# Kernel optimization log

Hardware: AMD Instinct MI355X
Metric: run time of the kernel (lower is better)

Reference implementation:

```python
import jax, jax.numpy as jnp
import numpy as np

D = 2048; HQ = 16; HKV = 4; HD = 128
E = 8; F = 2048; FS = 11008; TOPK = 2
B = 2; S = 1024
EPS = 1e-6
NEG = -1e9


def setup_inputs() -> dict:
    key = jax.random.key(0)
    ks = jax.random.split(key, 16)
    p = lambda k, shape: jax.random.normal(k, shape, jnp.float32) * 0.02
    # rotary tables (rotate-half convention): [S, HD]
    pos = jnp.arange(S, dtype=jnp.float32)[:, None]
    inv = 1.0 / (10000.0 ** (jnp.arange(0, HD, 2, dtype=jnp.float32) / HD))
    ang = pos * inv[None, :]
    cos = jnp.concatenate([jnp.cos(ang), jnp.cos(ang)], axis=-1)
    sin = jnp.concatenate([jnp.sin(ang), jnp.sin(ang)], axis=-1)
    return dict(
        x=jax.random.normal(ks[0], (B, S, D), jnp.float32),
        rope_cos=cos, rope_sin=sin,
        attn_norm_w=jnp.ones((D,), jnp.float32),
        ffn_norm_w=jnp.ones((D,), jnp.float32),
        wq=p(ks[1], (D, HQ * HD)), bq=jnp.zeros((HQ * HD,), jnp.float32),
        wk=p(ks[2], (D, HKV * HD)), bk=jnp.zeros((HKV * HD,), jnp.float32),
        wv=p(ks[3], (D, HKV * HD)), bv=jnp.zeros((HKV * HD,), jnp.float32),
        wo=p(ks[4], (HQ * HD, D)),
        router_w=p(ks[5], (D, E)),
        w_gate=p(ks[6], (E, D, F)), w_up=p(ks[7], (E, D, F)), w_down=p(ks[8], (E, F, D)),
        ws_gate=p(ks[9], (D, FS)), ws_up=p(ks[10], (D, FS)), ws_down=p(ks[11], (FS, D)),
    )


def rmsnorm(x, w):
    return x * jax.lax.rsqrt(jnp.mean(x * x, axis=-1, keepdims=True) + EPS) * w


def rotate_half(x):
    x1, x2 = jnp.split(x, 2, axis=-1)
    return jnp.concatenate([-x2, x1], axis=-1)


def reference(x, rope_cos, rope_sin, attn_norm_w, ffn_norm_w,
              wq, bq, wk, bk, wv, bv, wo, router_w,
              w_gate, w_up, w_down, ws_gate, ws_up, ws_down):
    b, s, d = x.shape
    # ---- attention sublayer ----
    h = rmsnorm(x, attn_norm_w)
    q = (h @ wq + bq).reshape(b, s, HQ, HD)
    k = (h @ wk + bk).reshape(b, s, HKV, HD)
    v = (h @ wv + bv).reshape(b, s, HKV, HD)
    cos = rope_cos[None, :, None, :]
    sin = rope_sin[None, :, None, :]
    q = q * cos + rotate_half(q) * sin
    k = k * cos + rotate_half(k) * sin
    rep = HQ // HKV
    k = jnp.repeat(k, rep, axis=2)   # [b,s,HQ,HD]
    v = jnp.repeat(v, rep, axis=2)
    scores = jnp.einsum('bqhd,bkhd->bhqk', q, k) / np.sqrt(HD).astype(np.float32)
    causal = jnp.tril(jnp.ones((s, s), bool))
    scores = jnp.where(causal[None, None], scores, NEG)
    attn = jax.nn.softmax(scores, axis=-1)
    o = jnp.einsum('bhqk,bkhd->bqhd', attn, v).reshape(b, s, HQ * HD) @ wo
    new_k, new_v = k, v
    x = x + o
    # ---- MoE sublayer ----
    hn = rmsnorm(x, ffn_norm_w).reshape(b * s, d)   # [T,D]
    logits = hn @ router_w                           # [T,E]
    probs = jax.nn.softmax(logits, axis=-1)
    topv, topi = jax.lax.top_k(probs, TOPK)          # [T,K]
    topv = topv / jnp.sum(topv, axis=-1, keepdims=True)
    onehot = jax.nn.one_hot(topi, E, dtype=hn.dtype)  # [T,K,E]
    wdense = jnp.einsum('tke,tk->te', onehot, topv)   # sparse combine weights [T,E]
    g = jnp.einsum('td,edf->tef', hn, w_gate)
    u = jnp.einsum('td,edf->tef', hn, w_up)
    y = jnp.einsum('tef,efd->ted', jax.nn.silu(g) * u, w_down)
    routed = jnp.einsum('ted,te->td', y, wdense)
    shared = (jax.nn.silu(hn @ ws_gate) * (hn @ ws_up)) @ ws_down
    moe = (routed + shared).reshape(b, s, d)
    # load-balancing aux loss (Switch/Mixtral convention)
    frac = jnp.mean(onehot, axis=(0, 1))             # fraction dispatched per expert
    pmean = jnp.mean(probs, axis=0)
    aux_loss = E * jnp.sum(frac * pmean)
    out = x + moe
    return out, (new_k, new_v), aux_loss
```

## Files before the change

kernel.cpp:

```cpp
#include <hip/hip_runtime.h>

typedef unsigned short u16;
typedef unsigned int u32;
typedef unsigned long long u64;
typedef __attribute__((ext_vector_type(4))) unsigned short u16x4;
typedef __attribute__((ext_vector_type(8))) unsigned short u16x8;
typedef __attribute__((ext_vector_type(4))) float f32x4;
typedef __attribute__((ext_vector_type(8))) __bf16 bf16x8;

#define DD 2048
#define TT 2048
#define FSH 11008

__device__ __forceinline__ float bf2f(u16 u) {
  union { u32 i; float f; } v; v.i = ((u32)u) << 16; return v.f;
}
__device__ __forceinline__ u16 f2bf(float f) {
  union { float f; u32 i; } v; v.f = f;
  u32 r = v.i + 0x7fffu + ((v.i >> 16) & 1u);
  return (u16)(r >> 16);
}
__device__ __forceinline__ void gld16(const void* g, void* l) {
  __builtin_amdgcn_global_load_lds((const __attribute__((address_space(1))) void*)g,
                                   (__attribute__((address_space(3))) void*)l, 16, 0, 0);
}

#define MFMA16(d, a, b) d = __builtin_amdgcn_mfma_f32_16x16x32_bf16(a, b, d, 0, 0, 0)

__global__ __launch_bounds__(256) void rmsnorm_k(const float* __restrict__ x,
                                                 const float* __restrict__ w,
                                                 u16* __restrict__ out) {
  const int t = threadIdx.x;
  const float* xr = x + (size_t)blockIdx.x * DD;
  float4 a = *(const float4*)(xr + t * 8);
  float4 b = *(const float4*)(xr + t * 8 + 4);
  float ss = a.x*a.x + a.y*a.y + a.z*a.z + a.w*a.w
           + b.x*b.x + b.y*b.y + b.z*b.z + b.w*b.w;
#pragma unroll
  for (int m = 1; m < 64; m <<= 1) ss += __shfl_xor(ss, m);
  __shared__ float red[4];
  if ((t & 63) == 0) red[t >> 6] = ss;
  __syncthreads();
  float sc = rsqrtf((red[0] + red[1] + red[2] + red[3]) * (1.f / DD) + 1e-6f);
  float4 wa = *(const float4*)(w + t * 8);
  float4 wb = *(const float4*)(w + t * 8 + 4);
  u16x8 o;
  o[0] = f2bf(a.x * sc * wa.x); o[1] = f2bf(a.y * sc * wa.y);
  o[2] = f2bf(a.z * sc * wa.z); o[3] = f2bf(a.w * sc * wa.w);
  o[4] = f2bf(b.x * sc * wb.x); o[5] = f2bf(b.y * sc * wb.y);
  o[6] = f2bf(b.z * sc * wb.z); o[7] = f2bf(b.w * sc * wb.w);
  *(u16x8*)(out + (size_t)blockIdx.x * DD + t * 8) = o;
}

__global__ __launch_bounds__(256) void transp_k(const float* __restrict__ W,
                                                u16* __restrict__ Wt, int R, int C) {
  __shared__ u16 tile[64 * 80];
  const size_t msz = (size_t)R * C;
  const float* Wm = W + msz * blockIdx.z;
  u16* Wtm = Wt + msz * blockIdx.z;
  const int t = threadIdx.x;
  const int n0 = blockIdx.x * 64, k0 = blockIdx.y * 64;
#pragma unroll
  for (int p = 0; p < 4; ++p) {
    const int kk = (t >> 4) + p * 16;
    const int nn = (t & 15) * 4;
    float4 v = *(const float4*)(Wm + (size_t)(k0 + kk) * C + n0 + nn);
    tile[(nn + 0) * 80 + kk] = f2bf(v.x);
    tile[(nn + 1) * 80 + kk] = f2bf(v.y);
    tile[(nn + 2) * 80 + kk] = f2bf(v.z);
    tile[(nn + 3) * 80 + kk] = f2bf(v.w);
  }
  __syncthreads();
#pragma unroll
  for (int p = 0; p < 2; ++p) {
    const int n = (t >> 3) + p * 32;
    const int c = t & 7;
    u16x8 v = *(const u16x8*)(tile + n * 80 + c * 8);
    *(u16x8*)(Wtm + (size_t)(n0 + n) * R + k0 + c * 8) = v;
  }
}

template <int EPI, bool EXPERT, bool INDIR, bool SPLITK>
__global__ __launch_bounds__(256) void gemm2(
    const u16* __restrict__ A, const u16* __restrict__ Bt, void* __restrict__ Cp,
    const void* __restrict__ aux, const float* __restrict__ slotw,
    const int* __restrict__ slot_tok, const int* __restrict__ tiletab,
    int M, int N, int K, int Kc) {
  __shared__ u16 lA[128 * 32];
  __shared__ u16 lB[128 * 32];
  const int t = threadIdx.x, w = t >> 6, l = t & 63;
  const int n0 = blockIdx.x * 128;
  int m0;
  if constexpr (EXPERT) {
    const int ntil = tiletab[0];
    if ((int)blockIdx.y >= ntil) return;
    const int e = tiletab[1 + blockIdx.y * 2];
    m0 = tiletab[2 + blockIdx.y * 2];
    Bt += (size_t)e * N * K;
  } else {
    m0 = blockIdx.y * 128;
  }
  int kbase = 0, KC = K;
  if constexpr (SPLITK) { kbase = blockIdx.z * Kc; KC = Kc; }
  const int srow = w * 16 + (l >> 2);
  const int scol = (l & 3) * 8;
  const int r0 = m0 + srow, r1 = m0 + srow + 64;
  const u16 *ag0, *ag1;
  if constexpr (INDIR) {
    ag0 = A + (size_t)slot_tok[r0] * K + scol + kbase;
    ag1 = A + (size_t)slot_tok[r1] * K + scol + kbase;
  } else {
    ag0 = A + (size_t)r0 * K + scol + kbase;
    ag1 = A + (size_t)r1 * K + scol + kbase;
  }
  const u16* bg0 = Bt + (size_t)(n0 + srow) * K + scol + kbase;
  const u16* bg1 = Bt + (size_t)(n0 + srow + 64) * K + scol + kbase;
  u16* la = lA + w * 512;
  u16* lb = lB + w * 512;
  const int l15 = l & 15, l4 = l >> 4;
  const int wm = w >> 1, wn = w & 1;
  const int fa = (wm * 64 + l15) * 32 + l4 * 8;
  const int fb = (wn * 64 + l15) * 32 + l4 * 8;
  f32x4 acc[4][4] = {};
  for (int ko = 0; ko < KC; ko += 32) {
    __syncthreads();
    gld16(ag0 + ko, la);
    gld16(ag1 + ko, la + 2048);
    gld16(bg0 + ko, lb);
    gld16(bg1 + ko, lb + 2048);
    asm volatile("s_waitcnt vmcnt(0)" ::: "memory");
    __syncthreads();
    bf16x8 af[4], bf[4];
#pragma unroll
    for (int i = 0; i < 4; ++i) {
      af[i] = *(const bf16x8*)(lA + fa + i * 512);
      bf[i] = *(const bf16x8*)(lB + fb + i * 512);
    }
#pragma unroll
    for (int mi = 0; mi < 4; ++mi)
#pragma unroll
      for (int ni = 0; ni < 4; ++ni)
        MFMA16(acc[mi][ni], af[mi], bf[ni]);
  }
  float* Cf = (float*)Cp;
  if constexpr (SPLITK) Cf += (size_t)blockIdx.z * M * N;
#pragma unroll
  for (int mi = 0; mi < 4; ++mi) {
#pragma unroll
    for (int r = 0; r < 4; ++r) {
      const int row = m0 + wm * 64 + mi * 16 + l4 * 4 + r;
#pragma unroll
      for (int ni = 0; ni < 4; ++ni) {
        const int col = n0 + wn * 64 + ni * 16 + l15;
        const size_t idx = (size_t)row * N + col;
        const float v = acc[mi][ni][r];
        if constexpr (EPI == 0) Cf[idx] = v;
        else if constexpr (EPI == 2) ((u16*)Cp)[idx] = f2bf(v);
        else if constexpr (EPI == 3) {
          const float g = bf2f(((const u16*)aux)[idx]);
          ((u16*)Cp)[idx] = f2bf(v * g / (1.f + __expf(-g)));
        } else {
          ((u16*)Cp)[idx] = f2bf(slotw[row] * v);
        }
      }
    }
  }
}

template <int EPI, bool SPLITK>
__global__ __launch_bounds__(512, 2) void gemm8(
    const u16* __restrict__ A, const u16* __restrict__ Bt, void* __restrict__ Cp,
    const u16* __restrict__ aux, int M, int N, int K, int Kc) {
  __shared__ char lds[131072];
  const int t = threadIdx.x, w = t >> 6, l = t & 63;
  const int gx = gridDim.x;
  const int nwg = gx * gridDim.y;
  int wg = blockIdx.y * gx + blockIdx.x;
  wg = (wg & 7) * (nwg >> 3) + (wg >> 3);
  const int n0 = (wg % gx) * 256;
  const int m0 = (wg / gx) * 256;
  int kbase = 0, KC = K;
  if constexpr (SPLITK) {
    kbase = blockIdx.z * Kc;
    const int rem = K - kbase;
    KC = rem < Kc ? rem : Kc;
  }
  const int ktiles = KC >> 6;
  const int wm = w >> 2, wn = w & 3;
  const int l15 = l & 15, l4 = l >> 4;
  const int sro = l >> 3, sc = l & 7;

  const u16* sgp[2][2][2];
  u32 sdo[2][2][2];
#pragma unroll
  for (int isB = 0; isB < 2; ++isB)
#pragma unroll
    for (int h = 0; h < 2; ++h)
#pragma unroll
      for (int i = 0; i < 2; ++i) {
        const int q = i * 8 + w;
        const int r0 = isB ? (((q >> 2) << 6) + h * 32 + (q & 3) * 8)
                           : (((q & 8) << 4) + h * 64 + (q & 7) * 8);
        const int r = r0 + sro;
        const int cl = sc ^ (r & 7);
        const u16* base = isB ? (Bt + (size_t)(n0 + r) * K) : (A + (size_t)(m0 + r) * K);
        sgp[isB][h][i] = base + kbase + cl * 8;
        sdo[isB][h][i] = (u32)(isB * 32768 + r0 * 128);
      }
  auto stage = [&](int b, int isB, int h, int kt) {
    const int kk = kt < ktiles ? kt : ktiles - 1;
#pragma unroll
    for (int i = 0; i < 2; ++i)
      gld16(sgp[isB][h][i] + kk * 64, lds + b * 65536 + sdo[isB][h][i]);
  };
  auto ldA = [&](int b, int mi, int ks) {
    const int row = wm * 128 + mi * 16 + l15;
    const int ch = (ks * 4 + l4) ^ (row & 7);
    return *(const bf16x8*)(lds + b * 65536 + row * 128 + ch * 16);
  };
  auto ldB = [&](int b, int ni, int ks) {
    const int row = wn * 64 + ni * 16 + l15;
    const int ch = (ks * 4 + l4) ^ (row & 7);
    return *(const bf16x8*)(lds + b * 65536 + 32768 + row * 128 + ch * 16);
  };

  f32x4 acc[8][4] = {};
  bf16x8 aR[4][2], b0[2][2], b1[2][2];

  stage(0, 0, 0, 0); stage(0, 1, 0, 0); stage(0, 1, 1, 0); stage(0, 0, 1, 0);
  stage(1, 0, 0, 1); stage(1, 1, 1, 1); stage(1, 0, 1, 1);
  asm volatile("s_waitcnt vmcnt(6)" ::: "memory");
  __builtin_amdgcn_s_barrier();

  for (int kt = 0; kt < ktiles; kt += 2) {
#pragma unroll
    for (int mi = 0; mi < 4; ++mi) { aR[mi][0] = ldA(0, mi, 0); aR[mi][1] = ldA(0, mi, 1); }
#pragma unroll
    for (int ni = 0; ni < 2; ++ni) { b0[ni][0] = ldB(0, ni, 0); b0[ni][1] = ldB(0, ni, 1); }
    stage(1, 1, 0, kt + 1);
    __builtin_amdgcn_s_barrier();
    asm volatile("s_waitcnt lgkmcnt(0)" ::: "memory");
    __builtin_amdgcn_s_setprio(1);
#pragma unroll
    for (int mi = 0; mi < 4; ++mi)
#pragma unroll
      for (int ni = 0; ni < 2; ++ni) {
        MFMA16(acc[mi][ni], aR[mi][0], b0[ni][0]);
        MFMA16(acc[mi][ni], aR[mi][1], b0[ni][1]);
      }
    __builtin_amdgcn_s_setprio(0);
    __builtin_amdgcn_s_barrier();
#pragma unroll
    for (int ni = 0; ni < 2; ++ni) { b1[ni][0] = ldB(0, ni + 2, 0); b1[ni][1] = ldB(0, ni + 2, 1); }
    stage(0, 0, 0, kt + 2);
    __builtin_amdgcn_s_barrier();
    asm volatile("s_waitcnt lgkmcnt(0)" ::: "memory");
    __builtin_amdgcn_s_setprio(1);
#pragma unroll
    for (int mi = 0; mi < 4; ++mi)
#pragma unroll
      for (int ni = 0; ni < 2; ++ni) {
        MFMA16(acc[mi][ni + 2], aR[mi][0], b1[ni][0]);
        MFMA16(acc[mi][ni + 2], aR[mi][1], b1[ni][1]);
      }
    __builtin_amdgcn_s_setprio(0);
    __builtin_amdgcn_s_barrier();
#pragma unroll
    for (int mi = 0; mi < 4; ++mi) { aR[mi][0] = ldA(0, mi + 4, 0); aR[mi][1] = ldA(0, mi + 4, 1); }
    stage(0, 1, 1, kt + 2);
    __builtin_amdgcn_s_barrier();
    asm volatile("s_waitcnt lgkmcnt(0)" ::: "memory");
    __builtin_amdgcn_s_setprio(1);
#pragma unroll
    for (int mi = 0; mi < 4; ++mi)
#pragma unroll
      for (int ni = 0; ni < 2; ++ni) {
        MFMA16(acc[mi + 4][ni + 2], aR[mi][0], b1[ni][0]);
        MFMA16(acc[mi + 4][ni + 2], aR[mi][1], b1[ni][1]);
      }
    __builtin_amdgcn_s_setprio(0);
    __builtin_amdgcn_s_barrier();
    stage(0, 0, 1, kt + 2);
    __builtin_amdgcn_s_barrier();
    __builtin_amdgcn_s_setprio(1);
#pragma unroll
    for (int mi = 0; mi < 4; ++mi)
#pragma unroll
      for (int ni = 0; ni < 2; ++ni) {
        MFMA16(acc[mi + 4][ni], aR[mi][0], b0[ni][0]);
        MFMA16(acc[mi + 4][ni], aR[mi][1], b0[ni][1]);
      }
    __builtin_amdgcn_s_setprio(0);
    asm volatile("s_waitcnt vmcnt(6)" ::: "memory");
    __builtin_amdgcn_s_barrier();
#pragma unroll
    for (int mi = 0; mi < 4; ++mi) { aR[mi][0] = ldA(1, mi, 0); aR[mi][1] = ldA(1, mi, 1); }
#pragma unroll
    for (int ni = 0; ni < 2; ++ni) { b0[ni][0] = ldB(1, ni, 0); b0[ni][1] = ldB(1, ni, 1); }
    stage(0, 1, 0, kt + 2);
    __builtin_amdgcn_s_barrier();
    asm volatile("s_waitcnt lgkmcnt(0)" ::: "memory");
    __builtin_amdgcn_s_setprio(1);
#pragma unroll
    for (int mi = 0; mi < 4; ++mi)
#pragma unroll
      for (int ni = 0; ni < 2; ++ni) {
        MFMA16(acc[mi][ni], aR[mi][0], b0[ni][0]);
        MFMA16(acc[mi][ni], aR[mi][1], b0[ni][1]);
      }
    __builtin_amdgcn_s_setprio(0);
    __builtin_amdgcn_s_barrier();
#pragma unroll
    for (int ni = 0; ni < 2; ++ni) { b1[ni][0] = ldB(1, ni + 2, 0); b1[ni][1] = ldB(1, ni + 2, 1); }
    stage(1, 0, 0, kt + 3);
    __builtin_amdgcn_s_barrier();
    asm volatile("s_waitcnt lgkmcnt(0)" ::: "memory");
    __builtin_amdgcn_s_setprio(1);
#pragma unroll
    for (int mi = 0; mi < 4; ++mi)
#pragma unroll
      for (int ni = 0; ni < 2; ++ni) {
        MFMA16(acc[mi][ni + 2], aR[mi][0], b1[ni][0]);
        MFMA16(acc[mi][ni + 2], aR[mi][1], b1[ni][1]);
      }
    __builtin_amdgcn_s_setprio(0);
    __builtin_amdgcn_s_barrier();
#pragma unroll
    for (int mi = 0; mi < 4; ++mi) { aR[mi][0] = ldA(1, mi + 4, 0); aR[mi][1] = ldA(1, mi + 4, 1); }
    stage(1, 1, 1, kt + 3);
    __builtin_amdgcn_s_barrier();
    asm volatile("s_waitcnt lgkmcnt(0)" ::: "memory");
    __builtin_amdgcn_s_setprio(1);
#pragma unroll
    for (int mi = 0; mi < 4; ++mi)
#pragma unroll
      for (int ni = 0; ni < 2; ++ni) {
        MFMA16(acc[mi + 4][ni + 2], aR[mi][0], b1[ni][0]);
        MFMA16(acc[mi + 4][ni + 2], aR[mi][1], b1[ni][1]);
      }
    __builtin_amdgcn_s_setprio(0);
    __builtin_amdgcn_s_barrier();
    stage(1, 0, 1, kt + 3);
    __builtin_amdgcn_s_barrier();
    __builtin_amdgcn_s_setprio(1);
#pragma unroll
    for (int mi = 0; mi < 4; ++mi)
#pragma unroll
      for (int ni = 0; ni < 2; ++ni) {
        MFMA16(acc[mi + 4][ni], aR[mi][0], b0[ni][0]);
        MFMA16(acc[mi + 4][ni], aR[mi][1], b0[ni][1]);
      }
    __builtin_amdgcn_s_setprio(0);
    asm volatile("s_waitcnt vmcnt(6)" ::: "memory");
    __builtin_amdgcn_s_barrier();
  }

  u16* C16 = (u16*)Cp;
  float* Cf = (float*)Cp;
  if constexpr (EPI == 10) C16 += (size_t)blockIdx.z * ((size_t)M * N);
  if constexpr (EPI == 11) Cf += (size_t)blockIdx.z * ((size_t)M * N);
#pragma unroll
  for (int mi = 0; mi < 8; ++mi)
#pragma unroll
    for (int rr = 0; rr < 4; ++rr) {
      const int row = m0 + wm * 128 + mi * 16 + l4 * 4 + rr;
#pragma unroll
      for (int ni = 0; ni < 4; ++ni) {
        const int col = n0 + wn * 64 + ni * 16 + l15;
        const size_t idx = (size_t)row * N + col;
        const float v = acc[mi][ni][rr];
        if constexpr (EPI == 11) {
          Cf[idx] = v;
        } else if constexpr (EPI == 3) {
          const float g = bf2f(aux[idx]);
          C16[idx] = f2bf(v * g / (1.f + __expf(-g)));
        } else {
          C16[idx] = f2bf(v);
        }
      }
    }
}

template <int NP, bool ADDB>
__global__ __launch_bounds__(256) void red_k(float* __restrict__ dst,
                                             const float* __restrict__ base,
                                             const float* __restrict__ parts,
                                             int mn4) {
  const int i = blockIdx.x * 256 + threadIdx.x;
  float4 s;
  if constexpr (ADDB) s = ((const float4*)base)[i];
  else { s.x = s.y = s.z = s.w = 0.f; }
#pragma unroll
  for (int p = 0; p < NP; ++p) {
    const float4 v = ((const float4*)parts)[(size_t)p * mn4 + i];
    s.x += v.x; s.y += v.y; s.z += v.z; s.w += v.w;
  }
  ((float4*)dst)[i] = s;
}

__global__ __launch_bounds__(256) void redbf_k(float* __restrict__ dst,
                                               const float* __restrict__ base,
                                               const u16* __restrict__ parts) {
  const int i = blockIdx.x * 256 + threadIdx.x;
  float s[8];
  const float* bp = base + (size_t)i * 8;
#pragma unroll
  for (int j = 0; j < 8; ++j) s[j] = bp[j];
#pragma unroll
  for (int p = 0; p < 4; ++p) {
    u16x8 v = ((const u16x8*)parts)[(size_t)p * 524288 + i];
#pragma unroll
    for (int j = 0; j < 8; ++j) s[j] += bf2f(v[j]);
  }
  float* dp = dst + (size_t)i * 8;
#pragma unroll
  for (int j = 0; j < 8; ++j) dp[j] = s[j];
}

__global__ __launch_bounds__(256) void rope_k(
    const float* __restrict__ qkv, const float* __restrict__ cosb, const float* __restrict__ sinb,
    const float* __restrict__ bq, const float* __restrict__ bk, const float* __restrict__ bv,
    u16* __restrict__ QR, u16* __restrict__ KR, u16* __restrict__ VB,
    float* __restrict__ NK, float* __restrict__ NV) {
  const int s = blockIdx.x, b = blockIdx.y, t = threadIdx.x;
  const size_t tok = (size_t)b * 1024 + s;
  const float* row = qkv + tok * 3072;
  const float* cr = cosb + s * 128;
  const float* sr = sinb + s * 128;
  for (int i = t; i < 1024; i += 256) {
    const int h = i >> 6, d = i & 63;
    const float v1 = row[h * 128 + d] + bq[h * 128 + d];
    const float v2 = row[h * 128 + d + 64] + bq[h * 128 + d + 64];
    const float o1 = v1 * cr[d] - v2 * sr[d];
    const float o2 = v2 * cr[d + 64] + v1 * sr[d + 64];
    const size_t qb = (((size_t)(b * 16 + h)) * 1024 + s) * 128;
    QR[qb + d] = f2bf(o1);
    QR[qb + d + 64] = f2bf(o2);
  }
  {
    const int h = t >> 6, d = t & 63;
    const float v1 = row[2048 + h * 128 + d] + bk[h * 128 + d];
    const float v2 = row[2048 + h * 128 + d + 64] + bk[h * 128 + d + 64];
    const float o1 = v1 * cr[d] - v2 * sr[d];
    const float o2 = v2 * cr[d + 64] + v1 * sr[d + 64];
    const size_t kb = (((size_t)(b * 4 + h)) * 1024 + s) * 128;
    KR[kb + d] = f2bf(o1);
    KR[kb + d + 64] = f2bf(o2);
    const size_t ob = tok * 2048;
#pragma unroll
    for (int rep = 0; rep < 4; ++rep) {
      NK[ob + (h * 4 + rep) * 128 + d] = o1;
      NK[ob + (h * 4 + rep) * 128 + d + 64] = o2;
    }
  }
  for (int i = t; i < 512; i += 256) {
    const int h = i >> 7, d = i & 127;
    const float v = row[2560 + i] + bv[i];
    VB[(((size_t)(b * 4 + h)) * 1024 + s) * 128 + d] = f2bf(v);
    const size_t ob = tok * 2048;
#pragma unroll
    for (int rep = 0; rep < 4; ++rep) NV[ob + (h * 4 + rep) * 128 + d] = v;
  }
}

__global__ __launch_bounds__(256) void attn_k(const u16* __restrict__ Q,
                                              const u16* __restrict__ Kc,
                                              const u16* __restrict__ Vc,
                                              u16* __restrict__ O) {
  const int qt = blockIdx.x, h = blockIdx.y, b = blockIdx.z;
  const int t = threadIdx.x, w = t >> 6, l = t & 63;
  const int kvh = h >> 2;
  __shared__ u16 Ks[64 * 128];
  __shared__ u16 Vt[128 * 66];
  __shared__ u16 Ps[4][16 * 68];
  const int l15 = l & 15, l4 = l >> 4;
  bf16x8 qf[4];
  {
    const u16* qb = Q + (((size_t)(b * 16 + h)) * 1024 + qt * 64 + w * 16 + l15) * 128 + l4 * 8;
#pragma unroll
    for (int c = 0; c < 4; ++c) qf[c] = *(const bf16x8*)(qb + c * 32);
  }
  float m_run[4] = {-1e30f, -1e30f, -1e30f, -1e30f};
  float l_run[4] = {0.f, 0.f, 0.f, 0.f};
  f32x4 accO[8] = {};
  const size_t kvbase = ((size_t)(b * 4 + kvh)) * 1024 * 128;
  const int ntiles = qt + 1;
  for (int kt = 0; kt < ntiles; ++kt) {
    __syncthreads();
    {
      const int key = t >> 2;
      const u16* kg = Kc + kvbase + (size_t)(kt * 64 + key) * 128;
      const u16* vg = Vc + kvbase + (size_t)(kt * 64 + key) * 128;
      const int sw = (key & 7) << 4;
#pragma unroll
      for (int p = 0; p < 4; ++p) {
        const int ch = (t & 3) * 4 + p;
        *(u16x8*)((char*)Ks + key * 256 + ((ch * 16) ^ sw)) = *(const u16x8*)(kg + ch * 8);
        const int d0 = ch * 8;
        u16x8 vv = *(const u16x8*)(vg + d0);
#pragma unroll
        for (int j = 0; j < 8; ++j) Vt[(d0 + j) * 66 + key] = vv[j];
      }
    }
    __syncthreads();
    f32x4 sf[4] = {};
#pragma unroll
    for (int nf = 0; nf < 4; ++nf) {
      const int keyl = nf * 16 + l15;
      const int sw = (keyl & 7) << 4;
      const char* kbase = (const char*)Ks + keyl * 256;
#pragma unroll
      for (int c = 0; c < 4; ++c) {
        bf16x8 kf = *(const bf16x8*)(kbase + ((c * 64 + l4 * 16) ^ sw));
        sf[nf] = __builtin_amdgcn_mfma_f32_16x16x32_bf16(qf[c], kf, sf[nf], 0, 0, 0);
      }
    }
    const int qg0 = qt * 64 + w * 16 + l4 * 4;
    float alpha[4];
#pragma unroll
    for (int r = 0; r < 4; ++r) {
      const int qg = qg0 + r;
      float tm = -1e30f;
#pragma unroll
      for (int nf = 0; nf < 4; ++nf) {
        const int kg = kt * 64 + nf * 16 + l15;
        float sv = sf[nf][r] * 0.088388347648318447f;
        sv = (kg <= qg) ? sv : -1e30f;
        sf[nf][r] = sv;
        tm = fmaxf(tm, sv);
      }
#pragma unroll
      for (int mm = 1; mm < 16; mm <<= 1) tm = fmaxf(tm, __shfl_xor(tm, mm));
      const float mn = fmaxf(m_run[r], tm);
      alpha[r] = __expf(m_run[r] - mn);
      m_run[r] = mn;
      float rs = 0.f;
#pragma unroll
      for (int nf = 0; nf < 4; ++nf) {
        const float p = __expf(sf[nf][r] - mn);
        sf[nf][r] = p;
        rs += p;
      }
#pragma unroll
      for (int mm = 1; mm < 16; mm <<= 1) rs += __shfl_xor(rs, mm);
      l_run[r] = l_run[r] * alpha[r] + rs;
    }
#pragma unroll
    for (int nf = 0; nf < 8; ++nf)
#pragma unroll
      for (int r = 0; r < 4; ++r) accO[nf][r] *= alpha[r];
#pragma unroll
    for (int nf = 0; nf < 4; ++nf)
#pragma unroll
      for (int r = 0; r < 4; ++r)
        Ps[w][(l4 * 4 + r) * 68 + nf * 16 + l15] = f2bf(sf[nf][r]);
    __syncthreads();
#pragma unroll
    for (int kc = 0; kc < 2; ++kc) {
      const u16* pb = &Ps[w][0] + l15 * 68 + kc * 32 + l4 * 8;
      union { u16x4 q[2]; bf16x8 v; } pu;
      pu.q[0] = *(const u16x4*)pb;
      pu.q[1] = *(const u16x4*)(pb + 4);
#pragma unroll
      for (int nf = 0; nf < 8; ++nf) {
        const int dd = nf * 16 + l15;
        const u16* vp = &Vt[0] + dd * 66 + kc * 32 + l4 * 8;
        union { u32 u[4]; bf16x8 v; } vu;
        vu.u[0] = *(const u32*)(vp);
        vu.u[1] = *(const u32*)(vp + 2);
        vu.u[2] = *(const u32*)(vp + 4);
        vu.u[3] = *(const u32*)(vp + 6);
        accO[nf] = __builtin_amdgcn_mfma_f32_16x16x32_bf16(pu.v, vu.v, accO[nf], 0, 0, 0);
      }
    }
  }
  const int qg0 = qt * 64 + w * 16 + l4 * 4;
#pragma unroll
  for (int nf = 0; nf < 8; ++nf) {
    const int dd = nf * 16 + l15;
#pragma unroll
    for (int r = 0; r < 4; ++r) {
      const float o = accO[nf][r] / l_run[r];
      O[((size_t)(b * 1024 + qg0 + r)) * 2048 + h * 128 + dd] = f2bf(o);
    }
  }
}

__global__ __launch_bounds__(256) void router_k(
    const float* __restrict__ x2, const float* __restrict__ wn, const float* __restrict__ rw,
    int* __restrict__ topi2, float* __restrict__ topw2,
    int* __restrict__ counts, u64* __restrict__ pmean) {
  const int t = threadIdx.x, w = t >> 6, l = t & 63;
  const int tok = blockIdx.x * 4 + w;
  __shared__ int lc[8];
  __shared__ u64 lp[8];
  if (t < 8) { lc[t] = 0; lp[t] = 0ull; }
  __syncthreads();
  const float* xr = x2 + (size_t)tok * DD;
  float ss = 0.f;
#pragma unroll
  for (int i = 0; i < 8; ++i) {
    float4 v = *(const float4*)(xr + l * 32 + i * 4);
    ss += v.x * v.x + v.y * v.y + v.z * v.z + v.w * v.w;
  }
#pragma unroll
  for (int m = 1; m < 64; m <<= 1) ss += __shfl_xor(ss, m);
  const float sc = rsqrtf(ss * (1.f / DD) + 1e-6f);
  float acc[8] = {};
  for (int i = 0; i < 32; ++i) {
    const int d = l * 32 + i;
    const float hv = xr[d] * sc * wn[d];
    float4 r0 = *(const float4*)(rw + d * 8);
    float4 r1 = *(const float4*)(rw + d * 8 + 4);
    acc[0] += hv * r0.x; acc[1] += hv * r0.y; acc[2] += hv * r0.z; acc[3] += hv * r0.w;
    acc[4] += hv * r1.x; acc[5] += hv * r1.y; acc[6] += hv * r1.z; acc[7] += hv * r1.w;
  }
#pragma unroll
  for (int m = 1; m < 64; m <<= 1)
#pragma unroll
    for (int e = 0; e < 8; ++e) acc[e] += __shfl_xor(acc[e], m);
  if (l == 0) {
    float mx = acc[0];
#pragma unroll
    for (int e = 1; e < 8; ++e) mx = fmaxf(mx, acc[e]);
    float p[8], sum = 0.f;
#pragma unroll
    for (int e = 0; e < 8; ++e) { p[e] = __expf(acc[e] - mx); sum += p[e]; }
    const float inv = 1.f / sum;
#pragma unroll
    for (int e = 0; e < 8; ++e) p[e] *= inv;
    int e0 = 0; float v0 = p[0];
#pragma unroll
    for (int e = 1; e < 8; ++e) if (p[e] > v0) { v0 = p[e]; e0 = e; }
    int e1 = (e0 == 0) ? 1 : 0; float v1 = p[e1];
#pragma unroll
    for (int e = 0; e < 8; ++e) if (e != e0 && p[e] > v1) { v1 = p[e]; e1 = e; }
    const float wsum = v0 + v1;
    topi2[tok * 2] = e0; topi2[tok * 2 + 1] = e1;
    topw2[tok * 2] = v0 / wsum; topw2[tok * 2 + 1] = v1 / wsum;
    atomicAdd(&lc[e0], 1); atomicAdd(&lc[e1], 1);
#pragma unroll
    for (int e = 0; e < 8; ++e) atomicAdd(&lp[e], (u64)((double)p[e] * 4294967296.0));
  }
  __syncthreads();
  if (t < 8) {
    if (lc[t]) atomicAdd(&counts[t], lc[t]);
    if (lp[t]) atomicAdd(&pmean[t], lp[t]);
  }
}

__global__ __launch_bounds__(256) void zero_k(int* __restrict__ counts, u64* __restrict__ pmean,
                                              int* __restrict__ slot_tok, float* __restrict__ slot_w) {
  const int i = blockIdx.x * 256 + threadIdx.x;
  if (i < 5120) { slot_tok[i] = 0; slot_w[i] = 0.f; }
  if (i < 8) { counts[i] = 0; pmean[i] = 0ull; }
}

__global__ void scan_k(const int* __restrict__ counts, int* __restrict__ cursors,
                       int* __restrict__ tiletab, const u64* __restrict__ pmean,
                       float* __restrict__ auxout) {
  if (threadIdx.x == 0) {
    int off = 0, nt = 0;
    double aux = 0.0;
    for (int e = 0; e < 8; ++e) {
      cursors[e] = off;
      const int c = counts[e];
      const int nte = (c + 127) >> 7;
      for (int i = 0; i < nte; ++i) {
        tiletab[1 + nt * 2] = e;
        tiletab[2 + nt * 2] = off + i * 128;
        ++nt;
      }
      off += nte * 128;
      const double pm = ((double)pmean[e] / 4294967296.0) / 2048.0;
      aux += ((double)c / 4096.0) * pm;
    }
    tiletab[0] = nt;
    *auxout = (float)(8.0 * aux);
  }
}

__global__ __launch_bounds__(256) void assign_k(const int* __restrict__ topi2,
                                                const float* __restrict__ topw2,
                                                int* __restrict__ cursors,
                                                int* __restrict__ slot_tok,
                                                float* __restrict__ slot_w,
                                                int* __restrict__ tok_slot) {
  const int tok = blockIdx.x * 256 + threadIdx.x;
#pragma unroll
  for (int j = 0; j < 2; ++j) {
    const int e = topi2[tok * 2 + j];
    const int s = atomicAdd(&cursors[e], 1);
    slot_tok[s] = tok;
    slot_w[s] = topw2[tok * 2 + j];
    tok_slot[tok * 2 + j] = s;
  }
}

__global__ __launch_bounds__(256) void final_k(float* __restrict__ out,
                                               const u16* __restrict__ routed,
                                               const int* __restrict__ tok_slot) {
  const int tok = blockIdx.x, t = threadIdx.x;
  const int s0 = tok_slot[tok * 2], s1 = tok_slot[tok * 2 + 1];
  u16x8 a = ((const u16x8*)(routed + (size_t)s0 * DD))[t];
  u16x8 b = ((const u16x8*)(routed + (size_t)s1 * DD))[t];
  float* o = out + (size_t)tok * DD + t * 8;
  float4 o0 = *(const float4*)o;
  float4 o1 = *(const float4*)(o + 4);
  o0.x += bf2f(a[0]) + bf2f(b[0]); o0.y += bf2f(a[1]) + bf2f(b[1]);
  o0.z += bf2f(a[2]) + bf2f(b[2]); o0.w += bf2f(a[3]) + bf2f(b[3]);
  o1.x += bf2f(a[4]) + bf2f(b[4]); o1.y += bf2f(a[5]) + bf2f(b[5]);
  o1.z += bf2f(a[6]) + bf2f(b[6]); o1.w += bf2f(a[7]) + bf2f(b[7]);
  *(float4*)o = o0;
  *(float4*)(o + 4) = o1;
}

extern "C" void kernel_launch(void* const* d_in, const int* in_sizes, int n_in,
                              void* d_out, int out_size, void* d_ws, size_t ws_size,
                              hipStream_t stream) {
  (void)in_sizes; (void)n_in; (void)out_size; (void)ws_size;
  const float* x    = (const float*)d_in[0];
  const float* rc   = (const float*)d_in[1];
  const float* rs   = (const float*)d_in[2];
  const float* anw  = (const float*)d_in[3];
  const float* fnw  = (const float*)d_in[4];
  const float* wq   = (const float*)d_in[5];
  const float* bq   = (const float*)d_in[6];
  const float* wk   = (const float*)d_in[7];
  const float* bk   = (const float*)d_in[8];
  const float* wv   = (const float*)d_in[9];
  const float* bv   = (const float*)d_in[10];
  const float* wo   = (const float*)d_in[11];
  const float* rw   = (const float*)d_in[12];
  const float* wg   = (const float*)d_in[13];
  const float* wu   = (const float*)d_in[14];
  const float* wd   = (const float*)d_in[15];
  const float* wsg  = (const float*)d_in[16];
  const float* wsu  = (const float*)d_in[17];
  const float* wsd  = (const float*)d_in[18];

  const size_t MB = (size_t)1 << 20;
  char* ws = (char*)d_ws;
  float* X2  = (float*)(ws + 0);
  u16*   HN  = (u16*)(ws + 16 * MB);
  char*  SM  = ws + 24 * MB;
  char*  AR  = ws + 25 * MB;

  int*   CNT   = (int*)(SM);
  u64*   PM    = (u64*)(SM + 64);
  int*   CURS  = (int*)(SM + 256);
  int*   TILT  = (int*)(SM + 512);
  int*   TOPI  = (int*)(SM + 4096);
  float* TOPW  = (float*)(SM + 40960);
  int*   STOK  = (int*)(SM + 73728);
  float* SW    = (float*)(SM + 98304);
  int*   TSLOT = (int*)(SM + 131072);

  u16*   H      = (u16*)(AR);
  u16*   WTQ    = (u16*)(AR + 8 * MB);
  float* PARTSQ = (float*)(AR + 20 * MB);
  float* QKVF   = (float*)(AR + 68 * MB);
  u16*   QR    = (u16*)(AR);
  u16*   KR    = (u16*)(AR + 8 * MB);
  u16*   VBb   = (u16*)(AR + 10 * MB);
  u16*   ATTNO = (u16*)(AR + 12 * MB);
  u16*   WTO    = (u16*)(AR + 20 * MB);
  float* PARTSW = (float*)(AR + 28 * MB);
  u16*   WTS    = (u16*)(AR);
  u16*   G      = (u16*)(AR + 44 * MB);
  u16*   PARTSD = (u16*)(AR + 88 * MB);
  u16*   WTE    = (u16*)(AR);
  u16*   GEXP   = (u16*)(AR + 64 * MB);
  u16*   ROUTED = (u16*)(AR + 84 * MB);

  float* out  = (float*)d_out;
  float* NK   = out + 4194304;
  float* NV   = out + 2 * 4194304;
  float* AUXO = out + 3 * 4194304;

  const dim3 b256(256);
  const dim3 b512(512);

  rmsnorm_k<<<TT, b256, 0, stream>>>(x, anw, H);
  transp_k<<<dim3(32, 32, 1), b256, 0, stream>>>(wq, WTQ, 2048, 2048);
  transp_k<<<dim3(8, 32, 1), b256, 0, stream>>>(wk, WTQ + (size_t)2048 * 2048, 2048, 512);
  transp_k<<<dim3(8, 32, 1), b256, 0, stream>>>(wv, WTQ + (size_t)2560 * 2048, 2048, 512);
  gemm8<11, true><<<dim3(12, 8, 2), b512, 0, stream>>>(H, WTQ, PARTSQ, nullptr, TT, 3072, 2048, 1024);
  red_k<2, false><<<6144, b256, 0, stream>>>(QKVF, nullptr, PARTSQ, 1572864);
  rope_k<<<dim3(1024, 2), b256, 0, stream>>>(QKVF, rc, rs, bq, bk, bv, QR, KR, VBb, NK, NV);
  attn_k<<<dim3(16, 16, 2), b256, 0, stream>>>(QR, KR, VBb, ATTNO);
  transp_k<<<dim3(32, 32, 1), b256, 0, stream>>>(wo, WTO, 2048, 2048);
  gemm8<11, true><<<dim3(8, 8, 4), b512, 0, stream>>>(ATTNO, WTO, PARTSW, nullptr, TT, 2048, 2048, 512);
  red_k<4, true><<<4096, b256, 0, stream>>>(X2, x, PARTSW, 1048576);
  rmsnorm_k<<<TT, b256, 0, stream>>>(X2, fnw, HN);
  zero_k<<<20, b256, 0, stream>>>(CNT, PM, STOK, SW);
  router_k<<<512, b256, 0, stream>>>(X2, fnw, rw, TOPI, TOPW, CNT, PM);
  scan_k<<<1, 64, 0, stream>>>(CNT, CURS, TILT, PM, AUXO);
  assign_k<<<8, b256, 0, stream>>>(TOPI, TOPW, CURS, STOK, SW, TSLOT);
  transp_k<<<dim3(172, 32, 1), b256, 0, stream>>>(wsg, WTS, 2048, FSH);
  gemm8<2, false><<<dim3(43, 8, 1), b512, 0, stream>>>(HN, WTS, G, nullptr, TT, FSH, 2048, 2048);
  transp_k<<<dim3(172, 32, 1), b256, 0, stream>>>(wsu, WTS, 2048, FSH);
  gemm8<3, false><<<dim3(43, 8, 1), b512, 0, stream>>>(HN, WTS, G, G, TT, FSH, 2048, 2048);
  transp_k<<<dim3(32, 172, 1), b256, 0, stream>>>(wsd, WTS, FSH, 2048);
  gemm8<10, true><<<dim3(8, 8, 4), b512, 0, stream>>>(G, WTS, PARTSD, nullptr, TT, 2048, FSH, 2816);
  redbf_k<<<2048, b256, 0, stream>>>(out, X2, PARTSD);
  transp_k<<<dim3(32, 32, 8), b256, 0, stream>>>(wg, WTE, 2048, 2048);
  gemm2<2, true, true, false><<<dim3(16, 40, 1), b256, 0, stream>>>(
      HN, WTE, GEXP, nullptr, nullptr, STOK, TILT, 5120, 2048, 2048, 0);
  transp_k<<<dim3(32, 32, 8), b256, 0, stream>>>(wu, WTE, 2048, 2048);
  gemm2<3, true, true, false><<<dim3(16, 40, 1), b256, 0, stream>>>(
      HN, WTE, GEXP, GEXP, nullptr, STOK, TILT, 5120, 2048, 2048, 0);
  transp_k<<<dim3(32, 32, 8), b256, 0, stream>>>(wd, WTE, 2048, 2048);
  gemm2<4, true, false, false><<<dim3(16, 40, 1), b256, 0, stream>>>(
      GEXP, WTE, ROUTED, nullptr, SW, STOK, TILT, 5120, 2048, 2048, 0);
  final_k<<<TT, b256, 0, stream>>>(out, ROUTED, TSLOT);
}
```

Before: 990.9 us.

## Fuse shared-expert gate/up GEMMs with SiLU epilogue and fold QKV split-K reduction into rope

Adds a gemm_gu kernel that computes the shared-expert gate and up projections together, sharing the A tile, and writes silu(g)*u directly, processed in three column groups with chunked weight transposes. This removes the separate gate GEMM, the bf16 round trip of G, and one full pass over HN. The QKV split-K reduction kernel is dropped; rope now sums the two partial buffers itself. The gemm8 workgroup-to-tile mapping is changed to iterate M fastest, and the buffer layout is reorganised to fit the new scratch areas.

```diff
diff --git a/kernel.cpp b/kernel.cpp
--- a/kernel.cpp
+++ b/kernel.cpp
@@ -173,12 +173,12 @@
     const u16* __restrict__ aux, int M, int N, int K, int Kc) {
   __shared__ char lds[131072];
   const int t = threadIdx.x, w = t >> 6, l = t & 63;
-  const int gx = gridDim.x;
-  const int nwg = gx * gridDim.y;
+  const int gx = gridDim.x, gy = gridDim.y;
+  const int nwg = gx * gy;
   int wg = blockIdx.y * gx + blockIdx.x;
   wg = (wg & 7) * (nwg >> 3) + (wg >> 3);
-  const int n0 = (wg % gx) * 256;
-  const int m0 = (wg / gx) * 256;
+  const int m0 = (wg % gy) * 256;
+  const int n0 = (wg / gy) * 256;
   int kbase = 0, KC = K;
   if constexpr (SPLITK) {
     kbase = blockIdx.z * Kc;
@@ -381,6 +381,214 @@
     }
 }
 
+__global__ __launch_bounds__(512, 2) void gemm_gu(
+    const u16* __restrict__ A, const u16* __restrict__ Btg, const u16* __restrict__ Btu,
+    u16* __restrict__ act, int K, int LDC, int cg0) {
+  __shared__ char lds[131072];
+  const int t = threadIdx.x, w = t >> 6, l = t & 63;
+  const int gx = gridDim.x;
+  const int nwg = gx * 8;
+  int wg = blockIdx.y * gx + blockIdx.x;
+  wg = (wg & 7) * (nwg >> 3) + (wg >> 3);
+  const int m0 = (wg & 7) * 256;
+  const int nt = wg >> 3;
+  const int ktiles = K >> 6;
+  const int wm = w >> 2, wn = w & 3;
+  const int l15 = l & 15, l4 = l >> 4;
+  const int sro = l >> 3, sc = l & 7;
+
+  const u16* sga[2][2]; u32 sda[2][2];
+#pragma unroll
+  for (int h = 0; h < 2; ++h)
+#pragma unroll
+    for (int i = 0; i < 2; ++i) {
+      const int q = i * 8 + w;
+      const int r0 = ((q & 8) << 4) + h * 64 + (q & 7) * 8;
+      const int r = r0 + sro;
+      const int cl = sc ^ (r & 7);
+      sga[h][i] = A + (size_t)(m0 + r) * K + cl * 8;
+      sda[h][i] = (u32)(r0 * 128);
+    }
+  const u16* sgb[2][2]; u32 sdb[2][2];
+#pragma unroll
+  for (int mat = 0; mat < 2; ++mat)
+#pragma unroll
+    for (int i = 0; i < 2; ++i) {
+      const int q = i * 8 + w;
+      const int r0 = q * 8;
+      const int r = r0 + sro;
+      const int cl = sc ^ (r & 7);
+      const u16* B = mat ? Btu : Btg;
+      sgb[mat][i] = B + (size_t)(nt * 128 + r) * K + cl * 8;
+      sdb[mat][i] = (u32)(32768 + mat * 16384 + r0 * 128);
+    }
+  auto stgA = [&](int b, int h, int kt) {
+    const int kk = kt < ktiles ? kt : ktiles - 1;
+#pragma unroll
+    for (int i = 0; i < 2; ++i) gld16(sga[h][i] + kk * 64, lds + b * 65536 + sda[h][i]);
+  };
+  auto stgB = [&](int b, int mat, int kt) {
+    const int kk = kt < ktiles ? kt : ktiles - 1;
+#pragma unroll
+    for (int i = 0; i < 2; ++i) gld16(sgb[mat][i] + kk * 64, lds + b * 65536 + sdb[mat][i]);
+  };
+  auto ldA = [&](int b, int mi, int ks) {
+    const int row = wm * 128 + mi * 16 + l15;
+    const int ch = (ks * 4 + l4) ^ (row & 7);
+    return *(const bf16x8*)(lds + b * 65536 + row * 128 + ch * 16);
+  };
+  auto ldB = [&](int b, int mat, int ni, int ks) {
+    const int row = wn * 32 + ni * 16 + l15;
+    const int ch = (ks * 4 + l4) ^ (row & 7);
+    return *(const bf16x8*)(lds + b * 65536 + 32768 + mat * 16384 + row * 128 + ch * 16);
+  };
+
+  f32x4 accg[8][2] = {}, accu[8][2] = {};
+  bf16x8 aR[4][2], bg[2][2], bu[2][2];
+
+  stgA(0, 0, 0); stgB(0, 0, 0); stgB(0, 1, 0); stgA(0, 1, 0);
+  stgA(1, 0, 1); stgB(1, 1, 1); stgA(1, 1, 1);
+  asm volatile("s_waitcnt vmcnt(6)" ::: "memory");
+  __builtin_amdgcn_s_barrier();
+
+  for (int kt = 0; kt < ktiles; kt += 2) {
+#pragma unroll
+    for (int mi = 0; mi < 4; ++mi) { aR[mi][0] = ldA(0, mi, 0); aR[mi][1] = ldA(0, mi, 1); }
+#pragma unroll
+    for (int ni = 0; ni < 2; ++ni) { bg[ni][0] = ldB(0, 0, ni, 0); bg[ni][1] = ldB(0, 0, ni, 1); }
+    stgB(1, 0, kt + 1);
+    __builtin_amdgcn_s_barrier();
+    asm volatile("s_waitcnt lgkmcnt(0)" ::: "memory");
+    __builtin_amdgcn_s_setprio(1);
+#pragma unroll
+    for (int mi = 0; mi < 4; ++mi)
+#pragma unroll
+      for (int ni = 0; ni < 2; ++ni) {
+        MFMA16(accg[mi][ni], aR[mi][0], bg[ni][0]);
+        MFMA16(accg[mi][ni], aR[mi][1], bg[ni][1]);
+      }
+    __builtin_amdgcn_s_setprio(0);
+    __builtin_amdgcn_s_barrier();
+#pragma unroll
+    for (int ni = 0; ni < 2; ++ni) { bu[ni][0] = ldB(0, 1, ni, 0); bu[ni][1] = ldB(0, 1, ni, 1); }
+    stgA(0, 0, kt + 2);
+    __builtin_amdgcn_s_barrier();
+    asm volatile("s_waitcnt lgkmcnt(0)" ::: "memory");
+    __builtin_amdgcn_s_setprio(1);
+#pragma unroll
+    for (int mi = 0; mi < 4; ++mi)
+#pragma unroll
+      for (int ni = 0; ni < 2; ++ni) {
+        MFMA16(accu[mi][ni], aR[mi][0], bu[ni][0]);
+        MFMA16(accu[mi][ni], aR[mi][1], bu[ni][1]);
+      }
+    __builtin_amdgcn_s_setprio(0);
+    __builtin_amdgcn_s_barrier();
+#pragma unroll
+    for (int mi = 0; mi < 4; ++mi) { aR[mi][0] = ldA(0, mi + 4, 0); aR[mi][1] = ldA(0, mi + 4, 1); }
+    stgB(0, 1, kt + 2);
+    __builtin_amdgcn_s_barrier();
+    asm volatile("s_waitcnt lgkmcnt(0)" ::: "memory");
+    __builtin_amdgcn_s_setprio(1);
+#pragma unroll
+    for (int mi = 0; mi < 4; ++mi)
+#pragma unroll
+      for (int ni = 0; ni < 2; ++ni) {
+        MFMA16(accu[mi + 4][ni], aR[mi][0], bu[ni][0]);
+        MFMA16(accu[mi + 4][ni], aR[mi][1], bu[ni][1]);
+      }
+    __builtin_amdgcn_s_setprio(0);
+    __builtin_amdgcn_s_barrier();
+    stgA(0, 1, kt + 2);
+    __builtin_amdgcn_s_barrier();
+    __builtin_amdgcn_s_setprio(1);
+#pragma unroll
+    for (int mi = 0; mi < 4; ++mi)
+#pragma unroll
+      for (int ni = 0; ni < 2; ++ni) {
+        MFMA16(accg[mi + 4][ni], aR[mi][0], bg[ni][0]);
+        MFMA16(accg[mi + 4][ni], aR[mi][1], bg[ni][1]);
+      }
+    __builtin_amdgcn_s_setprio(0);
+    asm volatile("s_waitcnt vmcnt(6)" ::: "memory");
+    __builtin_amdgcn_s_barrier();
+#pragma unroll
+    for (int mi = 0; mi < 4; ++mi) { aR[mi][0] = ldA(1, mi, 0); aR[mi][1] = ldA(1, mi, 1); }
+#pragma unroll
+    for (int ni = 0; ni < 2; ++ni) { bg[ni][0] = ldB(1, 0, ni, 0); bg[ni][1] = ldB(1, 0, ni, 1); }
+    stgB(0, 0, kt + 2);
+    __builtin_amdgcn_s_barrier();
+    asm volatile("s_waitcnt lgkmcnt(0)" ::: "memory");
+    __builtin_amdgcn_s_setprio(1);
+#pragma unroll
+    for (int mi = 0; mi < 4; ++mi)
+#pragma unroll
+      for (int ni = 0; ni < 2; ++ni) {
+        MFMA16(accg[mi][ni], aR[mi][0], bg[ni][0]);
+        MFMA16(accg[mi][ni], aR[mi][1], bg[ni][1]);
+      }
+    __builtin_amdgcn_s_setprio(0);
+    __builtin_amdgcn_s_barrier();
+#pragma unroll
+    for (int ni = 0; ni < 2; ++ni) { bu[ni][0] = ldB(1, 1, ni, 0); bu[ni][1] = ldB(1, 1, ni, 1); }
+    stgA(1, 0, kt + 3);
+    __builtin_amdgcn_s_barrier();
+    asm volatile("s_waitcnt lgkmcnt(0)" ::: "memory");
+    __builtin_amdgcn_s_setprio(1);
+#pragma unroll
+    for (int mi = 0; mi < 4; ++mi)
+#pragma unroll
+      for (int ni = 0; ni < 2; ++ni) {
+        MFMA16(accu[mi][ni], aR[mi][0], bu[ni][0]);
+        MFMA16(accu[mi][ni], aR[mi][1], bu[ni][1]);
+      }
+    __builtin_amdgcn_s_setprio(0);
+    __builtin_amdgcn_s_barrier();
+#pragma unroll
+    for (int mi = 0; mi < 4; ++mi) { aR[mi][0] = ldA(1, mi + 4, 0); aR[mi][1] = ldA(1, mi + 4, 1); }
+    stgB(1, 1, kt + 3);
+    __builtin_amdgcn_s_barrier();
+    asm volatile("s_waitcnt lgkmcnt(0)" ::: "memory");
+    __builtin_amdgcn_s_setprio(1);
+#pragma unroll
+    for (int mi = 0; mi < 4; ++mi)
+#pragma unroll
+      for (int ni = 0; ni < 2; ++ni) {
+        MFMA16(accu[mi + 4][ni], aR[mi][0], bu[ni][0]);
+        MFMA16(accu[mi + 4][ni], aR[mi][1], bu[ni][1]);
+      }
+    __builtin_amdgcn_s_setprio(0);
+    __builtin_amdgcn_s_barrier();
+    stgA(1, 1, kt + 3);
+    __builtin_amdgcn_s_barrier();
+    __builtin_amdgcn_s_setprio(1);
+#pragma unroll
+    for (int mi = 0; mi < 4; ++mi)
+#pragma unroll
+      for (int ni = 0; ni < 2; ++ni) {
+        MFMA16(accg[mi + 4][ni], aR[mi][0], bg[ni][0]);
+        MFMA16(accg[mi + 4][ni], aR[mi][1], bg[ni][1]);
+      }
+    __builtin_amdgcn_s_setprio(0);
+    asm volatile("s_waitcnt vmcnt(6)" ::: "memory");
+    __builtin_amdgcn_s_barrier();
+  }
+
+#pragma unroll
+  for (int mi = 0; mi < 8; ++mi)
+#pragma unroll
+    for (int rr = 0; rr < 4; ++rr) {
+      const int row = m0 + wm * 128 + mi * 16 + l4 * 4 + rr;
+#pragma unroll
+      for (int ni = 0; ni < 2; ++ni) {
+        const int col = cg0 + nt * 128 + wn * 32 + ni * 16 + l15;
+        const float g = accg[mi][ni][rr];
+        const float u = accu[mi][ni][rr];
+        act[(size_t)row * LDC + col] = f2bf(u * g / (1.f + __expf(-g)));
+      }
+    }
+}
+
 template <int NP, bool ADDB>
 __global__ __launch_bounds__(256) void red_k(float* __restrict__ dst,
                                              const float* __restrict__ base,
@@ -418,19 +626,21 @@
 }
 
 __global__ __launch_bounds__(256) void rope_k(
-    const float* __restrict__ qkv, const float* __restrict__ cosb, const float* __restrict__ sinb,
+    const float* __restrict__ p0, const float* __restrict__ p1,
+    const float* __restrict__ cosb, const float* __restrict__ sinb,
     const float* __restrict__ bq, const float* __restrict__ bk, const float* __restrict__ bv,
     u16* __restrict__ QR, u16* __restrict__ KR, u16* __restrict__ VB,
     float* __restrict__ NK, float* __restrict__ NV) {
   const int s = blockIdx.x, b = blockIdx.y, t = threadIdx.x;
   const size_t tok = (size_t)b * 1024 + s;
-  const float* row = qkv + tok * 3072;
+  const float* r0 = p0 + tok * 3072;
+  const float* r1 = p1 + tok * 3072;
   const float* cr = cosb + s * 128;
   const float* sr = sinb + s * 128;
   for (int i = t; i < 1024; i += 256) {
     const int h = i >> 6, d = i & 63;
-    const float v1 = row[h * 128 + d] + bq[h * 128 + d];
-    const float v2 = row[h * 128 + d + 64] + bq[h * 128 + d + 64];
+    const float v1 = r0[h * 128 + d] + r1[h * 128 + d] + bq[h * 128 + d];
+    const float v2 = r0[h * 128 + d + 64] + r1[h * 128 + d + 64] + bq[h * 128 + d + 64];
     const float o1 = v1 * cr[d] - v2 * sr[d];
     const float o2 = v2 * cr[d + 64] + v1 * sr[d + 64];
     const size_t qb = (((size_t)(b * 16 + h)) * 1024 + s) * 128;
@@ -439,8 +649,8 @@
   }
   {
     const int h = t >> 6, d = t & 63;
-    const float v1 = row[2048 + h * 128 + d] + bk[h * 128 + d];
-    const float v2 = row[2048 + h * 128 + d + 64] + bk[h * 128 + d + 64];
+    const float v1 = r0[2048 + h * 128 + d] + r1[2048 + h * 128 + d] + bk[h * 128 + d];
+    const float v2 = r0[2048 + h * 128 + d + 64] + r1[2048 + h * 128 + d + 64] + bk[h * 128 + d + 64];
     const float o1 = v1 * cr[d] - v2 * sr[d];
     const float o2 = v2 * cr[d + 64] + v1 * sr[d + 64];
     const size_t kb = (((size_t)(b * 4 + h)) * 1024 + s) * 128;
@@ -455,7 +665,7 @@
   }
   for (int i = t; i < 512; i += 256) {
     const int h = i >> 7, d = i & 127;
-    const float v = row[2560 + i] + bv[i];
+    const float v = r0[2560 + i] + r1[2560 + i] + bv[i];
     VB[(((size_t)(b * 4 + h)) * 1024 + s) * 128 + d] = f2bf(v);
     const size_t ob = tok * 2048;
 #pragma unroll
@@ -759,16 +969,17 @@
   u16*   H      = (u16*)(AR);
   u16*   WTQ    = (u16*)(AR + 8 * MB);
   float* PARTSQ = (float*)(AR + 20 * MB);
-  float* QKVF   = (float*)(AR + 68 * MB);
-  u16*   QR    = (u16*)(AR);
-  u16*   KR    = (u16*)(AR + 8 * MB);
-  u16*   VBb   = (u16*)(AR + 10 * MB);
-  u16*   ATTNO = (u16*)(AR + 12 * MB);
-  u16*   WTO    = (u16*)(AR + 20 * MB);
-  float* PARTSW = (float*)(AR + 28 * MB);
-  u16*   WTS    = (u16*)(AR);
-  u16*   G      = (u16*)(AR + 44 * MB);
-  u16*   PARTSD = (u16*)(AR + 88 * MB);
+  u16*   ATTNO = (u16*)(AR);
+  u16*   QR    = (u16*)(AR + 68 * MB);
+  u16*   KR    = (u16*)(AR + 76 * MB);
+  u16*   VBb   = (u16*)(AR + 78 * MB);
+  u16*   WTO    = (u16*)(AR + 8 * MB);
+  float* PARTSW = (float*)(AR + 16 * MB);
+  u16*   G      = (u16*)(AR);
+  u16*   WTSg   = (u16*)(AR + 43 * MB);
+  u16*   WTSu   = (u16*)(AR + 59 * MB);
+  u16*   WTSd   = (u16*)(AR + 43 * MB);
+  u16*   PARTSD = (u16*)(AR + 86 * MB);
   u16*   WTE    = (u16*)(AR);
   u16*   GEXP   = (u16*)(AR + 64 * MB);
   u16*   ROUTED = (u16*)(AR + 84 * MB);
@@ -786,8 +997,8 @@
   transp_k<<<dim3(8, 32, 1), b256, 0, stream>>>(wk, WTQ + (size_t)2048 * 2048, 2048, 512);
   transp_k<<<dim3(8, 32, 1), b256, 0, stream>>>(wv, WTQ + (size_t)2560 * 2048, 2048, 512);
   gemm8<11, true><<<dim3(12, 8, 2), b512, 0, stream>>>(H, WTQ, PARTSQ, nullptr, TT, 3072, 2048, 1024);
-  red_k<2, false><<<6144, b256, 0, stream>>>(QKVF, nullptr, PARTSQ, 1572864);
-  rope_k<<<dim3(1024, 2), b256, 0, stream>>>(QKVF, rc, rs, bq, bk, bv, QR, KR, VBb, NK, NV);
+  rope_k<<<dim3(1024, 2), b256, 0, stream>>>(PARTSQ, PARTSQ + (size_t)TT * 3072, rc, rs,
+                                             bq, bk, bv, QR, KR, VBb, NK, NV);
   attn_k<<<dim3(16, 16, 2), b256, 0, stream>>>(QR, KR, VBb, ATTNO);
   transp_k<<<dim3(32, 32, 1), b256, 0, stream>>>(wo, WTO, 2048, 2048);
   gemm8<11, true><<<dim3(8, 8, 4), b512, 0, stream>>>(ATTNO, WTO, PARTSW, nullptr, TT, 2048, 2048, 512);
@@ -797,12 +1008,17 @@
   router_k<<<512, b256, 0, stream>>>(X2, fnw, rw, TOPI, TOPW, CNT, PM);
   scan_k<<<1, 64, 0, stream>>>(CNT, CURS, TILT, PM, AUXO);
   assign_k<<<8, b256, 0, stream>>>(TOPI, TOPW, CURS, STOK, SW, TSLOT);
-  transp_k<<<dim3(172, 32, 1), b256, 0, stream>>>(wsg, WTS, 2048, FSH);
-  gemm8<2, false><<<dim3(43, 8, 1), b512, 0, stream>>>(HN, WTS, G, nullptr, TT, FSH, 2048, 2048);
-  transp_k<<<dim3(172, 32, 1), b256, 0, stream>>>(wsu, WTS, 2048, FSH);
-  gemm8<3, false><<<dim3(43, 8, 1), b512, 0, stream>>>(HN, WTS, G, G, TT, FSH, 2048, 2048);
-  transp_k<<<dim3(32, 172, 1), b256, 0, stream>>>(wsd, WTS, FSH, 2048);
-  gemm8<10, true><<<dim3(8, 8, 4), b512, 0, stream>>>(G, WTS, PARTSD, nullptr, TT, 2048, FSH, 2816);
+  {
+    const int cg[4] = {0, 3712, 7424, 11008};
+    for (int gi = 0; gi < 3; ++gi) {
+      const int c0 = cg[gi], wgrp = cg[gi + 1] - c0, ngc = wgrp >> 7;
+      transp_k<<<dim3(wgrp / 64, 32, 1), b256, 0, stream>>>(wsg + c0, WTSg, 2048, FSH);
+      transp_k<<<dim3(wgrp / 64, 32, 1), b256, 0, stream>>>(wsu + c0, WTSu, 2048, FSH);
+      gemm_gu<<<dim3(ngc, 8, 1), b512, 0, stream>>>(HN, WTSg, WTSu, G, 2048, FSH, c0);
+    }
+  }
+  transp_k<<<dim3(32, 172, 1), b256, 0, stream>>>(wsd, WTSd, FSH, 2048);
+  gemm8<10, true><<<dim3(8, 8, 4), b512, 0, stream>>>(G, WTSd, PARTSD, nullptr, TT, 2048, FSH, 2816);
   redbf_k<<<2048, b256, 0, stream>>>(out, X2, PARTSD);
   transp_k<<<dim3(32, 32, 8), b256, 0, stream>>>(wg, WTE, 2048, 2048);
   gemm2<2, true, true, false><<<dim3(16, 40, 1), b256, 0, stream>>>(
```

After: 936.2 us. 5.5% less time.
